# Kernel tuning notes

Hardware: AMD Instinct MI355X
Metric: run time of the kernel (lower is better)

Reference implementation:

```python
import jax, jax.numpy as jnp
import numpy as np

NUM_NODES = 100000
EMB_DIM = 256
HID_DIM = 256
NUM_REL = 500
NUM_EDGES = 250000


def setup_inputs() -> dict:
    key = jax.random.key(0)
    ks = jax.random.split(key, 6)
    x = jax.random.normal(ks[0], (NUM_NODES, EMB_DIM), dtype=jnp.float32)
    edge_index = jax.random.randint(ks[1], (2, NUM_EDGES), 0, NUM_NODES, dtype=jnp.int64)
    edge_type = jax.random.randint(ks[2], (NUM_EDGES,), 0, NUM_REL, dtype=jnp.int64)
    # nn.Linear weights: shape [out, in]; _init_weights -> normal(0,1), bias zero
    W_head = jax.random.normal(ks[3], (HID_DIM, EMB_DIM), dtype=jnp.float32)
    b_head = jnp.zeros((HID_DIM,), dtype=jnp.float32)
    W_tail = jax.random.normal(ks[4], (HID_DIM, EMB_DIM), dtype=jnp.float32)
    b_tail = jnp.zeros((HID_DIM,), dtype=jnp.float32)
    rel_emb = jax.random.normal(ks[5], (NUM_REL, HID_DIM), dtype=jnp.float32)
    return {"x": x, "edge_index": edge_index, "edge_type": edge_type,
            "W_head": W_head, "b_head": b_head,
            "W_tail": W_tail, "b_tail": b_tail, "rel_emb": rel_emb}


def reference(x, edge_index, edge_type, W_head, b_head, W_tail, b_tail, rel_emb):
    # gcn == 'no' branch of DistMultNet.forward
    h_head = x[edge_index[0]] @ W_head.T + b_head          # [E, H]
    h_tail = x[edge_index[1]] @ W_tail.T + b_tail          # [E, H]
    h_rel = rel_emb[edge_type]                             # [E, H]
    scores = jnp.sum(h_head * h_rel * h_tail, axis=1)      # [E]
    return jax.nn.sigmoid(scores)
```

## Files before the change

kernel.cpp:

```cpp
#include <hip/hip_runtime.h>
#include <math.h>

#define EMB 256

typedef _Float16 half8 __attribute__((ext_vector_type(8)));
typedef float f32x4 __attribute__((ext_vector_type(4)));

__device__ __forceinline__ void gload_lds16(const void* gsrc, void* lds) {
    __builtin_amdgcn_global_load_lds(
        (const __attribute__((address_space(1))) void*)gsrc,
        (__attribute__((address_space(3))) void*)lds,
        16, 0, 0);
}

__device__ __forceinline__ void split8(const f32x4 a, const f32x4 b,
                                       half8& hi, half8& lo) {
#pragma unroll
    for (int i = 0; i < 4; ++i) {
        hi[i]     = (_Float16)a[i];
        lo[i]     = (_Float16)(a[i] - (float)hi[i]);
        hi[4 + i] = (_Float16)b[i];
        lo[4 + i] = (_Float16)(b[i] - (float)hi[4 + i]);
    }
}

__global__ void presplit_w(const float* __restrict__ Wh, const float* __restrict__ Wt,
                           _Float16* __restrict__ Whs, _Float16* __restrict__ Wts)
{
    const int g = blockIdx.x * 256 + threadIdx.x;
    const int m = g >> 5;
    const int cs = g & 31;
    const int c = cs >> 2, seg = cs & 3;
    const float* src = (m < 256) ? Wh : Wt;
    _Float16* dst    = (m < 256) ? Whs : Wts;
    const int r = m & 255;

    const float* s = src + (size_t)r * EMB + c * 32 + seg * 8;
    const f32x4 v0 = *(const f32x4*)s;
    const f32x4 v1 = *(const f32x4*)(s + 4);
    half8 hi, lo;
    split8(v0, v1, hi, lo);
    _Float16* d = dst + (size_t)r * 512 + c * 64;
    const int sw = r & 7;
    *(half8*)(d + ((seg       ^ sw) << 3)) = hi;
    *(half8*)(d + (((4 + seg) ^ sw) << 3)) = lo;
}

__global__ __launch_bounds__(256, 4)
void gemm_dual(const float* __restrict__ X,
               const _Float16* __restrict__ Whs, const _Float16* __restrict__ Wts,
               const float* __restrict__ bh, const float* __restrict__ bt,
               float* __restrict__ Hout, float* __restrict__ Tout,
               int M, int nwg)
{
    __shared__ __align__(16) _Float16 Ax[128 * 64];
    __shared__ __align__(16) _Float16 Bh[128 * 64];
    __shared__ __align__(16) _Float16 Bt[128 * 64];

    const int fl = blockIdx.x;
    const int q = nwg >> 3, r = nwg & 7;
    const int xcd = fl & 7, ix = fl >> 3;
    const int wg = (xcd < r) ? xcd * (q + 1) + ix
                             : r * (q + 1) + (xcd - r) * q + ix;
    const int n0 = (wg & 1) << 7;
    const int m0 = (wg >> 1) << 7;

    const int tid = threadIdx.x;
    const int lane = tid & 63;
    const int wv = tid >> 6;
    const int wm = (wv >> 1) << 6;
    const int wn = (wv & 1) << 6;
    const int l15 = lane & 15, l4 = lane >> 4;

    const int ar = tid >> 1;
    const int ahalf = tid & 1;
    const int gmA = m0 + ar;
    const float* aSrc = X + (size_t)(gmA < M ? gmA : M - 1) * EMB + ahalf * 16;
    char* aDst = (char*)Ax + ar * 128;
    const int ar7 = ar & 7;
    const int s0 = ahalf * 2, s1 = s0 + 1;
    const int oh0 = ((s0       ^ ar7) << 4), ol0 = (((4 + s0) ^ ar7) << 4);
    const int oh1 = ((s1       ^ ar7) << 4), ol1 = (((4 + s1) ^ ar7) << 4);

    const int brow = tid >> 3, bg = tid & 7;
    const char* bhSrc = (const char*)Whs + (size_t)(n0 + brow) * 1024 + bg * 16;
    const char* btSrc = (const char*)Wts + (size_t)(n0 + brow) * 1024 + bg * 16;
    char* bhDst = (char*)Bh + brow * 128 + bg * 16;
    char* btDst = (char*)Bt + brow * 128 + bg * 16;

    f32x4 accH[4][4], accT[4][4];
#pragma unroll
    for (int i = 0; i < 4; ++i)
#pragma unroll
        for (int j = 0; j < 4; ++j) {
            accH[i][j] = (f32x4){0.f, 0.f, 0.f, 0.f};
            accT[i][j] = (f32x4){0.f, 0.f, 0.f, 0.f};
        }

    f32x4 xg[4];
#pragma unroll
    for (int p = 0; p < 4; ++p) xg[p] = *(const f32x4*)(aSrc + p * 4);

    for (int c = 0; c < 8; ++c) {
        if (c) __syncthreads();
        const int cb = c << 7;
#pragma unroll
        for (int i = 0; i < 4; ++i) {
            gload_lds16(bhSrc + (size_t)i * 32768 + cb, bhDst + i * 4096);
            gload_lds16(btSrc + (size_t)i * 32768 + cb, btDst + i * 4096);
        }
        {
            half8 hi0, lo0, hi1, lo1;
            split8(xg[0], xg[1], hi0, lo0);
            split8(xg[2], xg[3], hi1, lo1);
            *(half8*)(aDst + oh0) = hi0;
            *(half8*)(aDst + ol0) = lo0;
            *(half8*)(aDst + oh1) = hi1;
            *(half8*)(aDst + ol1) = lo1;
        }
        __syncthreads();

        if (c < 7) {
            const float* an = aSrc + (c + 1) * 32;
#pragma unroll
            for (int p = 0; p < 4; ++p) xg[p] = *(const f32x4*)(an + p * 4);
        }

        half8 ahh[4], ahl[4];
#pragma unroll
        for (int fi = 0; fi < 4; ++fi) {
            const int row = wm + fi * 16 + l15;
            const char* rb = (const char*)Ax + row * 128;
            ahh[fi] = *(const half8*)(rb + (((l4    ) ^ (row & 7)) << 4));
            ahl[fi] = *(const half8*)(rb + (((l4 + 4) ^ (row & 7)) << 4));
        }
#pragma unroll
        for (int j = 0; j < 4; ++j) {
            const int n = wn + j * 16 + l15;
            const int n7 = n & 7;
            const char* hr = (const char*)Bh + n * 128;
            const char* tr = (const char*)Bt + n * 128;
            const half8 bhh = *(const half8*)(hr + (((l4    ) ^ n7) << 4));
            const half8 bhl = *(const half8*)(hr + (((l4 + 4) ^ n7) << 4));
            const half8 bth = *(const half8*)(tr + (((l4    ) ^ n7) << 4));
            const half8 btl = *(const half8*)(tr + (((l4 + 4) ^ n7) << 4));
#pragma unroll
            for (int i = 0; i < 4; ++i) {
                accH[i][j] = __builtin_amdgcn_mfma_f32_16x16x32_f16(ahh[i], bhh, accH[i][j], 0, 0, 0);
                accH[i][j] = __builtin_amdgcn_mfma_f32_16x16x32_f16(ahh[i], bhl, accH[i][j], 0, 0, 0);
                accH[i][j] = __builtin_amdgcn_mfma_f32_16x16x32_f16(ahl[i], bhh, accH[i][j], 0, 0, 0);
                accT[i][j] = __builtin_amdgcn_mfma_f32_16x16x32_f16(ahh[i], bth, accT[i][j], 0, 0, 0);
                accT[i][j] = __builtin_amdgcn_mfma_f32_16x16x32_f16(ahh[i], btl, accT[i][j], 0, 0, 0);
                accT[i][j] = __builtin_amdgcn_mfma_f32_16x16x32_f16(ahl[i], bth, accT[i][j], 0, 0, 0);
            }
        }
    }

    float bhv[4], btv[4];
#pragma unroll
    for (int j = 0; j < 4; ++j) {
        bhv[j] = bh[n0 + wn + j * 16 + l15];
        btv[j] = bt[n0 + wn + j * 16 + l15];
    }
#pragma unroll
    for (int i = 0; i < 4; ++i) {
        const int rbase = m0 + wm + i * 16 + l4 * 4;
#pragma unroll
        for (int rg = 0; rg < 4; ++rg) {
            const int gr = rbase + rg;
            if (gr < M) {
                float* dh = &Hout[(size_t)gr * EMB + n0 + wn];
                float* dt = &Tout[(size_t)gr * EMB + n0 + wn];
#pragma unroll
                for (int j = 0; j < 4; ++j) {
                    const int col = j * 16 + l15;
                    dh[col] = accH[i][j][rg] + bhv[j];
                    dt[col] = accT[i][j][rg] + btv[j];
                }
            }
        }
    }
}

__global__ __launch_bounds__(256)
void edge_score4(const float* __restrict__ H, const float* __restrict__ T,
                 const float* __restrict__ rel, const int* __restrict__ ei,
                 const int* __restrict__ et, float* __restrict__ out, int E)
{
    const int lane = threadIdx.x & 63;
    const int wid = threadIdx.x >> 6;
    const int base = (blockIdx.x * 4 + wid) * 4;
    if (base >= E) return;

    int e[4];
#pragma unroll
    for (int u = 0; u < 4; ++u) {
        int eu = base + u;
        e[u] = eu < E ? eu : E - 1;
    }

    const int lo = lane * 4;
    float4 h[4], t[4], g[4];
#pragma unroll
    for (int u = 0; u < 4; ++u) h[u] = *(const float4*)&H[(size_t)ei[e[u]] * EMB + lo];
#pragma unroll
    for (int u = 0; u < 4; ++u) t[u] = *(const float4*)&T[(size_t)ei[E + e[u]] * EMB + lo];
#pragma unroll
    for (int u = 0; u < 4; ++u) g[u] = *(const float4*)&rel[(size_t)et[e[u]] * EMB + lo];

    float p[4];
#pragma unroll
    for (int u = 0; u < 4; ++u)
        p[u] = h[u].x * g[u].x * t[u].x + h[u].y * g[u].y * t[u].y
             + h[u].z * g[u].z * t[u].z + h[u].w * g[u].w * t[u].w;

#pragma unroll
    for (int off = 32; off > 0; off >>= 1) {
#pragma unroll
        for (int u = 0; u < 4; ++u) p[u] += __shfl_xor(p[u], off, 64);
    }
    if (lane == 0) {
#pragma unroll
        for (int u = 0; u < 4; ++u)
            out[e[u]] = 1.0f / (1.0f + expf(-p[u]));
    }
}

__global__ __launch_bounds__(256)
void edge_direct(const float* __restrict__ X, const int* __restrict__ ei,
                 const int* __restrict__ et,
                 const float* __restrict__ Wh, const float* __restrict__ bh,
                 const float* __restrict__ Wt, const float* __restrict__ bt,
                 const float* __restrict__ rel, float* __restrict__ out, int E)
{
    __shared__ float xsrc[EMB], xdst[EMB];
    __shared__ float red[256];
    const int e = blockIdx.x;
    const int tid = threadIdx.x;
    const int src = ei[e], dst = ei[E + e], r = et[e];

    xsrc[tid] = X[(size_t)src * EMB + tid];
    xdst[tid] = X[(size_t)dst * EMB + tid];
    __syncthreads();

    float ah = 0.f, at = 0.f;
    const float* wh = Wh + (size_t)tid * EMB;
    const float* wt = Wt + (size_t)tid * EMB;
#pragma unroll 8
    for (int k = 0; k < EMB; k += 4) {
        float4 w4 = *(const float4*)&wh[k];
        ah += w4.x * xsrc[k] + w4.y * xsrc[k + 1] + w4.z * xsrc[k + 2] + w4.w * xsrc[k + 3];
        float4 v4 = *(const float4*)&wt[k];
        at += v4.x * xdst[k] + v4.y * xdst[k + 1] + v4.z * xdst[k + 2] + v4.w * xdst[k + 3];
    }
    red[tid] = (ah + bh[tid]) * rel[(size_t)r * EMB + tid] * (at + bt[tid]);
    __syncthreads();
    for (int s2 = 128; s2 > 0; s2 >>= 1) {
        if (tid < s2) red[tid] += red[tid + s2];
        __syncthreads();
    }
    if (tid == 0) out[e] = 1.0f / (1.0f + expf(-red[0]));
}

extern "C" void kernel_launch(void* const* d_in, const int* in_sizes, int n_in,
                              void* d_out, int out_size, void* d_ws, size_t ws_size,
                              hipStream_t stream) {
    const float* x   = (const float*)d_in[0];
    const int*   ei  = (const int*)d_in[1];
    const int*   et  = (const int*)d_in[2];
    const float* Wh  = (const float*)d_in[3];
    const float* bh  = (const float*)d_in[4];
    const float* Wt  = (const float*)d_in[5];
    const float* bt  = (const float*)d_in[6];
    const float* rel = (const float*)d_in[7];
    float* out = (float*)d_out;

    const int M = in_sizes[0] / EMB;
    const int E = in_sizes[2];

    const size_t szHT = (size_t)2 * M * EMB * sizeof(float);
    const size_t szWs = (size_t)2 * 256 * 512 * sizeof(_Float16);

    if (ws_size >= szHT + szWs) {
        float* H = (float*)d_ws;
        float* T = H + (size_t)M * EMB;
        _Float16* Whs = (_Float16*)((char*)d_ws + szHT);
        _Float16* Wts = Whs + (size_t)256 * 512;

        presplit_w<<<64, 256, 0, stream>>>(Wh, Wt, Whs, Wts);
        const int mtiles = (M + 127) / 128;
        const int nwg = 2 * mtiles;
        gemm_dual<<<nwg, 256, 0, stream>>>(x, Whs, Wts, bh, bt, H, T, M, nwg);
        edge_score4<<<(E + 15) / 16, 256, 0, stream>>>(H, T, rel, ei, et, out, E);
    } else {
        edge_direct<<<E, 256, 0, stream>>>(x, ei, et, Wh, bh, Wt, bt, rel, out, E);
    }
}
```

Before: 208.8 us.

## Double-buffer weight tiles in LDS and prefetch the next K-chunk asynchronously

The head and tail weight tiles now live in a two-slot LDS buffer. The next K-chunk is issued via global_load_lds before the current chunk's MFMAs run, so weight loads overlap compute instead of sitting between two barriers. Synchronisation moves to raw s_barrier with an explicit vmcnt/lgkmcnt wait and sched barriers. The larger LDS footprint lowers the occupancy hint from 4 to 2 blocks. The vmcnt(8) wait relies on load ordering and on the compiler's own waits for the X prefetch, which leaves a correctness and occupancy risk.

```diff
diff --git a/kernel.cpp b/kernel.cpp
--- a/kernel.cpp
+++ b/kernel.cpp
@@ -46,7 +46,7 @@
     *(half8*)(d + (((4 + seg) ^ sw) << 3)) = lo;
 }
 
-__global__ __launch_bounds__(256, 4)
+__global__ __launch_bounds__(256, 2)
 void gemm_dual(const float* __restrict__ X,
                const _Float16* __restrict__ Whs, const _Float16* __restrict__ Wts,
                const float* __restrict__ bh, const float* __restrict__ bt,
@@ -54,8 +54,7 @@
                int M, int nwg)
 {
     __shared__ __align__(16) _Float16 Ax[128 * 64];
-    __shared__ __align__(16) _Float16 Bh[128 * 64];
-    __shared__ __align__(16) _Float16 Bt[128 * 64];
+    __shared__ __align__(16) _Float16 Bd[2][2][128 * 64];
 
     const int fl = blockIdx.x;
     const int q = nwg >> 3, r = nwg & 7;
@@ -85,8 +84,7 @@
     const int brow = tid >> 3, bg = tid & 7;
     const char* bhSrc = (const char*)Whs + (size_t)(n0 + brow) * 1024 + bg * 16;
     const char* btSrc = (const char*)Wts + (size_t)(n0 + brow) * 1024 + bg * 16;
-    char* bhDst = (char*)Bh + brow * 128 + bg * 16;
-    char* btDst = (char*)Bt + brow * 128 + bg * 16;
+    const int bOff = brow * 128 + bg * 16;
 
     f32x4 accH[4][4], accT[4][4];
 #pragma unroll
@@ -97,18 +95,29 @@
             accT[i][j] = (f32x4){0.f, 0.f, 0.f, 0.f};
         }
 
+    auto STAGE_B = [&](int b, int c) {
+        const int cb = c << 7;
+#pragma unroll
+        for (int i = 0; i < 4; ++i) {
+            gload_lds16(bhSrc + (size_t)i * 32768 + cb,
+                        (char*)&Bd[b][0][0] + bOff + i * 4096);
+            gload_lds16(btSrc + (size_t)i * 32768 + cb,
+                        (char*)&Bd[b][1][0] + bOff + i * 4096);
+        }
+    };
+
     f32x4 xg[4];
 #pragma unroll
     for (int p = 0; p < 4; ++p) xg[p] = *(const f32x4*)(aSrc + p * 4);
+    STAGE_B(0, 0);
 
     for (int c = 0; c < 8; ++c) {
-        if (c) __syncthreads();
-        const int cb = c << 7;
-#pragma unroll
-        for (int i = 0; i < 4; ++i) {
-            gload_lds16(bhSrc + (size_t)i * 32768 + cb, bhDst + i * 4096);
-            gload_lds16(btSrc + (size_t)i * 32768 + cb, btDst + i * 4096);
-        }
+        __builtin_amdgcn_sched_barrier(0);
+        __builtin_amdgcn_s_barrier();
+        __builtin_amdgcn_sched_barrier(0);
+
+        if (c < 7) STAGE_B((c + 1) & 1, c + 1);
+
         {
             half8 hi0, lo0, hi1, lo1;
             split8(xg[0], xg[1], hi0, lo0);
@@ -118,13 +127,20 @@
             *(half8*)(aDst + oh1) = hi1;
             *(half8*)(aDst + ol1) = lo1;
         }
-        __syncthreads();
+
+        asm volatile("s_waitcnt vmcnt(8) lgkmcnt(0)" ::: "memory");
+        __builtin_amdgcn_sched_barrier(0);
+        __builtin_amdgcn_s_barrier();
+        __builtin_amdgcn_sched_barrier(0);
 
         if (c < 7) {
             const float* an = aSrc + (c + 1) * 32;
 #pragma unroll
             for (int p = 0; p < 4; ++p) xg[p] = *(const f32x4*)(an + p * 4);
         }
+
+        const char* BhB = (const char*)&Bd[c & 1][0][0];
+        const char* BtB = (const char*)&Bd[c & 1][1][0];
 
         half8 ahh[4], ahl[4];
 #pragma unroll
@@ -138,8 +154,8 @@
         for (int j = 0; j < 4; ++j) {
             const int n = wn + j * 16 + l15;
             const int n7 = n & 7;
-            const char* hr = (const char*)Bh + n * 128;
-            const char* tr = (const char*)Bt + n * 128;
+            const char* hr = BhB + n * 128;
+            const char* tr = BtB + n * 128;
             const half8 bhh = *(const half8*)(hr + (((l4    ) ^ n7) << 4));
             const half8 bhl = *(const half8*)(hr + (((l4 + 4) ^ n7) << 4));
             const half8 bth = *(const half8*)(tr + (((l4    ) ^ n7) << 4));
```

Result: faster. 183.3 us (-12.2%).

## Hold weight tiles in registers with persistent grid over M tiles

Applied to the files above, without the earlier changes.

Replaces the dual H/T GEMM with a persistent kernel of 512 blocks. Each block owns one 64-column slice of one weight matrix, keeps its hi/lo fp16 split in registers for the whole run, and loops over M tiles. The X tile is double-buffered in LDS, which drops the per-chunk weight reload into LDS and one barrier per chunk. The cost is that X is now re-read and re-split once per column slice (8 times instead of twice), and register pressure rises, which reduces occupancy to 2 blocks per CU.

```diff
diff --git a/kernel.cpp b/kernel.cpp
--- a/kernel.cpp
+++ b/kernel.cpp
@@ -5,13 +5,6 @@
 
 typedef _Float16 half8 __attribute__((ext_vector_type(8)));
 typedef float f32x4 __attribute__((ext_vector_type(4)));
-
-__device__ __forceinline__ void gload_lds16(const void* gsrc, void* lds) {
-    __builtin_amdgcn_global_load_lds(
-        (const __attribute__((address_space(1))) void*)gsrc,
-        (__attribute__((address_space(3))) void*)lds,
-        16, 0, 0);
-}
 
 __device__ __forceinline__ void split8(const f32x4 a, const f32x4 b,
                                        half8& hi, half8& lo) {
@@ -46,136 +39,121 @@
     *(half8*)(d + (((4 + seg) ^ sw) << 3)) = lo;
 }
 
-__global__ __launch_bounds__(256, 4)
-void gemm_dual(const float* __restrict__ X,
+__global__ __launch_bounds__(256, 2)
+void gemm_breg(const float* __restrict__ X,
                const _Float16* __restrict__ Whs, const _Float16* __restrict__ Wts,
                const float* __restrict__ bh, const float* __restrict__ bt,
                float* __restrict__ Hout, float* __restrict__ Tout,
-               int M, int nwg)
-{
-    __shared__ __align__(16) _Float16 Ax[128 * 64];
-    __shared__ __align__(16) _Float16 Bh[128 * 64];
-    __shared__ __align__(16) _Float16 Bt[128 * 64];
-
-    const int fl = blockIdx.x;
-    const int q = nwg >> 3, r = nwg & 7;
-    const int xcd = fl & 7, ix = fl >> 3;
-    const int wg = (xcd < r) ? xcd * (q + 1) + ix
-                             : r * (q + 1) + (xcd - r) * q + ix;
-    const int n0 = (wg & 1) << 7;
-    const int m0 = (wg >> 1) << 7;
+               int M, int mtiles)
+{
+    __shared__ __align__(16) _Float16 Axd[2][128 * 64];
+
+    const int bid = blockIdx.x;
+    const int slot = bid & 63;
+    const int v = bid >> 6;
+    const int mat = v >> 2;
+    const int n0g = (v & 3) << 6;
+
+    const _Float16* __restrict__ Ws = mat ? Wts : Whs;
+    const float* __restrict__ bias  = mat ? bt : bh;
+    float* __restrict__ OUT         = mat ? Tout : Hout;
 
     const int tid = threadIdx.x;
     const int lane = tid & 63;
     const int wv = tid >> 6;
     const int wm = (wv >> 1) << 6;
-    const int wn = (wv & 1) << 6;
+    const int wn = (wv & 1) << 5;
     const int l15 = lane & 15, l4 = lane >> 4;
+
+    half8 Bh_[2][8], Bl_[2][8];
+#pragma unroll
+    for (int j = 0; j < 2; ++j) {
+        const int row = n0g + wn + j * 16 + l15;
+        const char* rb = (const char*)Ws + (size_t)row * 1024;
+        const int r7 = row & 7;
+#pragma unroll
+        for (int c = 0; c < 8; ++c) {
+            Bh_[j][c] = *(const half8*)(rb + c * 128 + (((l4    ) ^ r7) << 4));
+            Bl_[j][c] = *(const half8*)(rb + c * 128 + (((l4 + 4) ^ r7) << 4));
+        }
+    }
+
+    float bv[2];
+#pragma unroll
+    for (int j = 0; j < 2; ++j) bv[j] = bias[n0g + wn + j * 16 + l15];
 
     const int ar = tid >> 1;
     const int ahalf = tid & 1;
-    const int gmA = m0 + ar;
-    const float* aSrc = X + (size_t)(gmA < M ? gmA : M - 1) * EMB + ahalf * 16;
-    char* aDst = (char*)Ax + ar * 128;
     const int ar7 = ar & 7;
     const int s0 = ahalf * 2, s1 = s0 + 1;
     const int oh0 = ((s0       ^ ar7) << 4), ol0 = (((4 + s0) ^ ar7) << 4);
     const int oh1 = ((s1       ^ ar7) << 4), ol1 = (((4 + s1) ^ ar7) << 4);
 
-    const int brow = tid >> 3, bg = tid & 7;
-    const char* bhSrc = (const char*)Whs + (size_t)(n0 + brow) * 1024 + bg * 16;
-    const char* btSrc = (const char*)Wts + (size_t)(n0 + brow) * 1024 + bg * 16;
-    char* bhDst = (char*)Bh + brow * 128 + bg * 16;
-    char* btDst = (char*)Bt + brow * 128 + bg * 16;
-
-    f32x4 accH[4][4], accT[4][4];
-#pragma unroll
-    for (int i = 0; i < 4; ++i)
-#pragma unroll
-        for (int j = 0; j < 4; ++j) {
-            accH[i][j] = (f32x4){0.f, 0.f, 0.f, 0.f};
-            accT[i][j] = (f32x4){0.f, 0.f, 0.f, 0.f};
+    for (int mt = slot; mt < mtiles; mt += 64) {
+        const int m0 = mt << 7;
+        const int gmA = m0 + ar;
+        const float* aSrc = X + (size_t)(gmA < M ? gmA : M - 1) * EMB + ahalf * 16;
+
+        f32x4 acc[4][2];
+#pragma unroll
+        for (int i = 0; i < 4; ++i)
+#pragma unroll
+            for (int j = 0; j < 2; ++j) acc[i][j] = (f32x4){0.f, 0.f, 0.f, 0.f};
+
+        f32x4 xg[4];
+#pragma unroll
+        for (int p = 0; p < 4; ++p) xg[p] = *(const f32x4*)(aSrc + p * 4);
+
+#pragma unroll
+        for (int c = 0; c < 8; ++c) {
+            {
+                char* aDst = (char*)&Axd[c & 1][0] + ar * 128;
+                half8 hi0, lo0, hi1, lo1;
+                split8(xg[0], xg[1], hi0, lo0);
+                split8(xg[2], xg[3], hi1, lo1);
+                *(half8*)(aDst + oh0) = hi0;
+                *(half8*)(aDst + ol0) = lo0;
+                *(half8*)(aDst + oh1) = hi1;
+                *(half8*)(aDst + ol1) = lo1;
+            }
+            __syncthreads();
+
+            if (c < 7) {
+                const float* an = aSrc + (c + 1) * 32;
+#pragma unroll
+                for (int p = 0; p < 4; ++p) xg[p] = *(const f32x4*)(an + p * 4);
+            }
+
+            const char* Ab = (const char*)&Axd[c & 1][0];
+            half8 ahh[4], ahl[4];
+#pragma unroll
+            for (int fi = 0; fi < 4; ++fi) {
+                const int row = wm + fi * 16 + l15;
+                const char* rb2 = Ab + row * 128;
+                ahh[fi] = *(const half8*)(rb2 + (((l4    ) ^ (row & 7)) << 4));
+                ahl[fi] = *(const half8*)(rb2 + (((l4 + 4) ^ (row & 7)) << 4));
+            }
+#pragma unroll
+            for (int j = 0; j < 2; ++j)
+#pragma unroll
+                for (int i = 0; i < 4; ++i) {
+                    acc[i][j] = __builtin_amdgcn_mfma_f32_16x16x32_f16(ahh[i], Bh_[j][c], acc[i][j], 0, 0, 0);
+                    acc[i][j] = __builtin_amdgcn_mfma_f32_16x16x32_f16(ahh[i], Bl_[j][c], acc[i][j], 0, 0, 0);
+                    acc[i][j] = __builtin_amdgcn_mfma_f32_16x16x32_f16(ahl[i], Bh_[j][c], acc[i][j], 0, 0, 0);
+                }
         }
 
-    f32x4 xg[4];
-#pragma unroll
-    for (int p = 0; p < 4; ++p) xg[p] = *(const f32x4*)(aSrc + p * 4);
-
-    for (int c = 0; c < 8; ++c) {
-        if (c) __syncthreads();
-        const int cb = c << 7;
 #pragma unroll
         for (int i = 0; i < 4; ++i) {
-            gload_lds16(bhSrc + (size_t)i * 32768 + cb, bhDst + i * 4096);
-            gload_lds16(btSrc + (size_t)i * 32768 + cb, btDst + i * 4096);
-        }
-        {
-            half8 hi0, lo0, hi1, lo1;
-            split8(xg[0], xg[1], hi0, lo0);
-            split8(xg[2], xg[3], hi1, lo1);
-            *(half8*)(aDst + oh0) = hi0;
-            *(half8*)(aDst + ol0) = lo0;
-            *(half8*)(aDst + oh1) = hi1;
-            *(half8*)(aDst + ol1) = lo1;
-        }
-        __syncthreads();
-
-        if (c < 7) {
-            const float* an = aSrc + (c + 1) * 32;
-#pragma unroll
-            for (int p = 0; p < 4; ++p) xg[p] = *(const f32x4*)(an + p * 4);
-        }
-
-        half8 ahh[4], ahl[4];
-#pragma unroll
-        for (int fi = 0; fi < 4; ++fi) {
-            const int row = wm + fi * 16 + l15;
-            const char* rb = (const char*)Ax + row * 128;
-            ahh[fi] = *(const half8*)(rb + (((l4    ) ^ (row & 7)) << 4));
-            ahl[fi] = *(const half8*)(rb + (((l4 + 4) ^ (row & 7)) << 4));
-        }
-#pragma unroll
-        for (int j = 0; j < 4; ++j) {
-            const int n = wn + j * 16 + l15;
-            const int n7 = n & 7;
-            const char* hr = (const char*)Bh + n * 128;
-            const char* tr = (const char*)Bt + n * 128;
-            const half8 bhh = *(const half8*)(hr + (((l4    ) ^ n7) << 4));
-            const half8 bhl = *(const half8*)(hr + (((l4 + 4) ^ n7) << 4));
-            const half8 bth = *(const half8*)(tr + (((l4    ) ^ n7) << 4));
-            const half8 btl = *(const half8*)(tr + (((l4 + 4) ^ n7) << 4));
-#pragma unroll
-            for (int i = 0; i < 4; ++i) {
-                accH[i][j] = __builtin_amdgcn_mfma_f32_16x16x32_f16(ahh[i], bhh, accH[i][j], 0, 0, 0);
-                accH[i][j] = __builtin_amdgcn_mfma_f32_16x16x32_f16(ahh[i], bhl, accH[i][j], 0, 0, 0);
-                accH[i][j] = __builtin_amdgcn_mfma_f32_16x16x32_f16(ahl[i], bhh, accH[i][j], 0, 0, 0);
-                accT[i][j] = __builtin_amdgcn_mfma_f32_16x16x32_f16(ahh[i], bth, accT[i][j], 0, 0, 0);
-                accT[i][j] = __builtin_amdgcn_mfma_f32_16x16x32_f16(ahh[i], btl, accT[i][j], 0, 0, 0);
-                accT[i][j] = __builtin_amdgcn_mfma_f32_16x16x32_f16(ahl[i], bth, accT[i][j], 0, 0, 0);
-            }
-        }
-    }
-
-    float bhv[4], btv[4];
-#pragma unroll
-    for (int j = 0; j < 4; ++j) {
-        bhv[j] = bh[n0 + wn + j * 16 + l15];
-        btv[j] = bt[n0 + wn + j * 16 + l15];
-    }
-#pragma unroll
-    for (int i = 0; i < 4; ++i) {
-        const int rbase = m0 + wm + i * 16 + l4 * 4;
-#pragma unroll
-        for (int rg = 0; rg < 4; ++rg) {
-            const int gr = rbase + rg;
-            if (gr < M) {
-                float* dh = &Hout[(size_t)gr * EMB + n0 + wn];
-                float* dt = &Tout[(size_t)gr * EMB + n0 + wn];
-#pragma unroll
-                for (int j = 0; j < 4; ++j) {
-                    const int col = j * 16 + l15;
-                    dh[col] = accH[i][j][rg] + bhv[j];
-                    dt[col] = accT[i][j][rg] + btv[j];
+            const int rbase = m0 + wm + i * 16 + l4 * 4;
+#pragma unroll
+            for (int rg = 0; rg < 4; ++rg) {
+                const int gr = rbase + rg;
+                if (gr < M) {
+                    float* dst = &OUT[(size_t)gr * EMB + n0g + wn];
+#pragma unroll
+                    for (int j = 0; j < 2; ++j)
+                        dst[j * 16 + l15] = acc[i][j][rg] + bv[j];
                 }
             }
         }
@@ -289,8 +267,7 @@
 
         presplit_w<<<64, 256, 0, stream>>>(Wh, Wt, Whs, Wts);
         const int mtiles = (M + 127) / 128;
-        const int nwg = 2 * mtiles;
-        gemm_dual<<<nwg, 256, 0, stream>>>(x, Whs, Wts, bh, bt, H, T, M, nwg);
+        gemm_breg<<<512, 256, 0, stream>>>(x, Whs, Wts, bh, bt, H, T, M, mtiles);
         edge_score4<<<(E + 15) / 16, 256, 0, stream>>>(H, T, rel, ei, et, out, E);
     } else {
         edge_direct<<<E, 256, 0, stream>>>(x, ei, et, Wh, bh, Wt, bt, rel, out, E);
```

Measured after the change: 230.1 us. 1.1x slower.
